# Optimization experiments

Measured on AMD Instinct MI355X. Metric: run time of the kernel, lower is better.

The kernel has to match this reference:

```python
import jax, jax.numpy as jnp
import numpy as np

BOS, EOS, MAX_STEPS = 1, 2, 50
VOCAB, EMBD, HID, CTX, SEQ = 50257, 512, 1024, 1024, 50


def setup_inputs() -> dict:
    key = jax.random.key(0)
    ks = jax.random.split(key, 13)
    s = 0.05
    return {
        "seq_enc_states": jax.random.normal(ks[0], (SEQ, 1, CTX), jnp.float32),
        "seq_enc_hidden": jax.random.normal(ks[1], (1, CTX), jnp.float32),
        "E": jax.random.normal(ks[2], (VOCAB, EMBD), jnp.float32) * s,
        "W_init": jax.random.normal(ks[3], (HID, CTX), jnp.float32) * s,
        "b_init": jax.random.normal(ks[4], (HID,), jnp.float32) * s,
        "Wa": jax.random.normal(ks[5], (CTX, HID), jnp.float32) * s,
        "ba": jax.random.normal(ks[6], (CTX,), jnp.float32) * s,
        "W_ih": jax.random.normal(ks[7], (3 * HID, EMBD + CTX), jnp.float32) * s,
        "W_hh": jax.random.normal(ks[8], (3 * HID, HID), jnp.float32) * s,
        "b_ih": jax.random.normal(ks[9], (3 * HID,), jnp.float32) * s,
        "b_hh": jax.random.normal(ks[10], (3 * HID,), jnp.float32) * s,
        "Wv": jax.random.normal(ks[11], (VOCAB, HID), jnp.float32) * s,
        "bv": jax.random.normal(ks[12], (VOCAB,), jnp.float32) * s,
    }


def _gru_cell(x, h, W_ih, W_hh, b_ih, b_hh):
    # torch.nn.GRUCell math
    gi = x @ W_ih.T + b_ih  # (1, 3H)
    gh = h @ W_hh.T + b_hh  # (1, 3H)
    i_r, i_z, i_n = jnp.split(gi, 3, axis=-1)
    h_r, h_z, h_n = jnp.split(gh, 3, axis=-1)
    r = jax.nn.sigmoid(i_r + h_r)
    z = jax.nn.sigmoid(i_z + h_z)
    n = jnp.tanh(i_n + r * h_n)
    return (1.0 - z) * n + z * h


def reference(seq_enc_states, seq_enc_hidden, E, W_init, b_init, Wa, ba,
              W_ih, W_hh, b_ih, b_hh, Wv, bv):
    enc = seq_enc_states[:, 0, :]                       # (S, CTX)
    h0 = seq_enc_hidden.reshape(1, -1) @ W_init.T + b_init  # (1, H)
    emb0 = E[BOS][None, :]                              # (1, EMBD)

    def step(carry, _):
        h, emb, done = carry
        # dot-product attention over the 50 encoder positions
        ph = h @ Wa.T + ba                              # (1, CTX)
        attn = jax.nn.softmax(ph @ enc.T, axis=-1)      # (1, S)
        ctx = attn @ enc                                # (1, CTX)
        x = jnp.concatenate([emb, ctx], axis=-1)        # (1, EMBD+CTX)
        h_new = _gru_cell(x, h, W_ih, W_hh, b_ih, b_hh)
        logp = jax.nn.log_softmax(h_new @ Wv.T + bv, axis=-1)  # (1, V)
        idx = jnp.argmax(logp[0])
        valid = jnp.logical_not(done)
        is_eos = idx == EOS
        emit_idx = jnp.where(valid & jnp.logical_not(is_eos), idx, -1).astype(jnp.int32)
        logp_out = jnp.where(valid, logp[0], 0.0)
        new_emb = jnp.where((valid & jnp.logical_not(is_eos))[..., None], E[idx][None, :], emb)
        new_h = jnp.where(valid, h_new, h)
        new_done = done | is_eos
        return (new_h, new_emb, new_done), (emit_idx, logp_out, valid)

    init = (h0, emb0, jnp.array(False))
    _, (indices, logps, valid) = jax.lax.scan(step, init, None, length=MAX_STEPS)
    # indices: (50,) int32, -1 where past eos / eos itself (not appended in original)
    return indices, logps, valid
```

## Files before the change

### kernel.cpp

```cpp
#include <hip/hip_runtime.h>
#include <hip/hip_fp8.h>
#include <cmath>

#define VOCABSZ 50257
#define EMBD 512
#define HIDD 1024
#define CTXD 1024
#define SEQL 50
#define NSTEPS 50
#define BOS_ID 1
#define EOS_ID 2

#define NTHR 256
#define NB_GH 768
#define NB_GI 768
#define NB_WR 64
#define NB_PRE (NB_GH + NB_GI + NB_WR)
#define NB_LOG 832
#define NW_LOG (NB_LOG * 4)
#define ST_STRIDE 12

#define OFF_M      0
#define OFF_T      51200
#define OFF_H      51264
#define OFF_CTX    53312
#define OFF_GI     54336
#define OFF_GH     57408
#define OFF_L      60480
#define OFF_STATS  110784
#define OFF_STATE  120768
#define OFF_WV8    120896

typedef float v2f __attribute__((ext_vector_type(2)));

__device__ __forceinline__ float wred_sum(float v) {
#pragma unroll
  for (int o = 32; o > 0; o >>= 1) v += __shfl_xor(v, o, 64);
  return v;
}

__device__ __forceinline__ float dot4(float4 a, float4 b) {
  return a.x * b.x + a.y * b.y + a.z * b.z + a.w * b.w;
}

__device__ __forceinline__ float wdot1024(const float* __restrict__ row, int lane,
                                          float4 b0, float4 b1, float4 b2, float4 b3) {
  const float4* r = (const float4*)row;
  float acc = dot4(r[lane], b0) + dot4(r[lane + 64], b1) +
              dot4(r[lane + 128], b2) + dot4(r[lane + 192], b3);
  return wred_sum(acc);
}

__device__ __forceinline__ bool beats(float v, int i, float v0, int i0) {
  return v > v0 || (v == v0 && i < i0);
}

__device__ __forceinline__ void top4_insert(float* v, int* ix, float w, int j) {
  if (!beats(w, j, v[3], ix[3])) return;
  v[3] = w; ix[3] = j;
#pragma unroll
  for (int k = 3; k > 0; --k) {
    if (beats(v[k], ix[k], v[k - 1], ix[k - 1])) {
      float tv = v[k]; v[k] = v[k - 1]; v[k - 1] = tv;
      int ti = ix[k]; ix[k] = ix[k - 1]; ix[k - 1] = ti;
    }
  }
}

#if __has_builtin(__builtin_amdgcn_cvt_pk_f32_fp8)
#define FP8_HW 1
#else
#define FP8_HW 0
__device__ __forceinline__ float fp8_sw(unsigned b) {
  unsigned s = b >> 7, e = (b >> 3) & 15, m = b & 7;
  float mag = (e == 0) ? ldexpf((float)m, -9) : ldexpf((float)(8 + m), (int)e - 10);
  return s ? -mag : mag;
}
#endif

__device__ __forceinline__ float acc16_fp8(uint4 a, const float* b) {
  float acc = 0.f;
  const unsigned dw[4] = {a.x, a.y, a.z, a.w};
#pragma unroll
  for (int d = 0; d < 4; ++d) {
#if FP8_HW
    v2f lo = __builtin_amdgcn_cvt_pk_f32_fp8((int)dw[d], false);
    v2f hi = __builtin_amdgcn_cvt_pk_f32_fp8((int)dw[d], true);
    acc += lo.x * b[d * 4 + 0] + lo.y * b[d * 4 + 1] +
           hi.x * b[d * 4 + 2] + hi.y * b[d * 4 + 3];
#else
    acc += fp8_sw(dw[d] & 0xff) * b[d * 4 + 0] +
           fp8_sw((dw[d] >> 8) & 0xff) * b[d * 4 + 1] +
           fp8_sw((dw[d] >> 16) & 0xff) * b[d * 4 + 2] +
           fp8_sw((dw[d] >> 24) & 0xff) * b[d * 4 + 3];
#endif
  }
  return acc;
}

__global__ void __launch_bounds__(NTHR)
k_cvt8(const float4* __restrict__ src, unsigned* __restrict__ dst, int n) {
  int i = blockIdx.x * NTHR + threadIdx.x;
  const int stride = gridDim.x * NTHR;
  for (; i < n; i += stride) {
    float4 v = src[i];
#if __has_builtin(__builtin_amdgcn_cvt_pk_fp8_f32)
    int p = 0;
    p = __builtin_amdgcn_cvt_pk_fp8_f32(v.x, v.y, p, false);
    p = __builtin_amdgcn_cvt_pk_fp8_f32(v.z, v.w, p, true);
    dst[i] = (unsigned)p;
#else
    __hip_fp8_e4m3 a(v.x), b(v.y), c(v.z), d(v.w);
    dst[i] = (unsigned)a.__x | ((unsigned)b.__x << 8) |
             ((unsigned)c.__x << 16) | ((unsigned)d.__x << 24);
#endif
  }
}

__global__ void __launch_bounds__(1024)
k0_matM(float* __restrict__ ws, const float* __restrict__ enc,
        const float* __restrict__ Wa) {
  const int kc = blockIdx.x;
  const int jg = blockIdx.y;
  const int tid = threadIdx.x;
  const int w = tid >> 6, lane = tid & 63;
  const int jw = w & 3, q = w >> 2;
  const int j = jg * 4 + jw;
  const int k = kc * 64 + lane;
  __shared__ float s_red[16][64];
  float acc0 = 0.f, acc1 = 0.f, acc2 = 0.f, acc3 = 0.f;
  if (j < SEQL) {
    const float4* e4 = (const float4*)(enc + (size_t)j * CTXD);
    const float* Wc = Wa + k;
    for (int c4 = q * 64; c4 < q * 64 + 64; ++c4) {
      float4 e = e4[c4];
      const float* wp = Wc + (size_t)(c4 * 4) * HIDD;
      acc0 += e.x * wp[0];
      acc1 += e.y * wp[HIDD];
      acc2 += e.z * wp[2 * HIDD];
      acc3 += e.w * wp[3 * HIDD];
    }
  }
  s_red[w][lane] = acc0 + acc1 + acc2 + acc3;
  __syncthreads();
  if (q == 0 && j < SEQL) {
    float v = s_red[jw][lane] + s_red[4 + jw][lane] +
              s_red[8 + jw][lane] + s_red[12 + jw][lane];
    ws[OFF_M + (size_t)j * HIDD + k] = v;
  }
}

__global__ void __launch_bounds__(NTHR)
k0_init(float* __restrict__ ws, const float* __restrict__ enc,
        const float* __restrict__ hid0, const float* __restrict__ Winit,
        const float* __restrict__ binit, const float* __restrict__ ba) {
  const int blk = blockIdx.x, tid = threadIdx.x;
  const int wave = tid >> 6, lane = tid & 63;
  if (blk == 0) {
    const float4* b4 = (const float4*)ba;
    float4 b0 = b4[lane], b1 = b4[lane + 64], b2 = b4[lane + 128], b3 = b4[lane + 192];
    for (int j = wave; j < SEQL; j += 4) {
      float v = wdot1024(enc + (size_t)j * CTXD, lane, b0, b1, b2, b3);
      if (lane == 0) ws[OFF_T + j] = v;
    }
    if (tid == 0) {
      int* st_emb = (int*)(ws + OFF_STATE);
      st_emb[0] = BOS_ID;
      st_emb[64] = 0;
    }
  } else {
    const float4* h4 = (const float4*)hid0;
    float4 b0 = h4[lane], b1 = h4[lane + 64], b2 = h4[lane + 128], b3 = h4[lane + 192];
    int row = (blk - 1) * 4 + wave;
    float v = wdot1024(Winit + (size_t)row * CTXD, lane, b0, b1, b2, b3) + binit[row];
    if (lane == 0) ws[OFF_H + row] = v;
  }
}

__global__ void __launch_bounds__(NTHR)
k_attn0(float* __restrict__ ws, const float* __restrict__ enc) {
  const int tid = threadIdx.x;
  const int wave = tid >> 6, lane = tid & 63;
  __shared__ float s_h[HIDD];
  __shared__ float s_sc[64], s_aw[64];
  ((float4*)s_h)[tid] = ((const float4*)(ws + OFF_H))[tid];
  __syncthreads();
  const float4* h4 = (const float4*)s_h;
  float4 b0 = h4[lane], b1 = h4[lane + 64], b2 = h4[lane + 128], b3 = h4[lane + 192];
  for (int j = wave; j < SEQL; j += 4) {
    float v = wdot1024(ws + OFF_M + (size_t)j * HIDD, lane, b0, b1, b2, b3) + ws[OFF_T + j];
    if (lane == 0) s_sc[j] = v;
  }
  __syncthreads();
  if (tid < 64) {
    float v = (tid < SEQL) ? s_sc[tid] : -INFINITY;
    float mx = v;
#pragma unroll
    for (int o = 32; o > 0; o >>= 1) mx = fmaxf(mx, __shfl_xor(mx, o, 64));
    float e = (tid < SEQL) ? expf(v - mx) : 0.f;
    float sm = wred_sum(e);
    if (tid < SEQL) s_aw[tid] = e / sm;
  }
  __syncthreads();
  const float4* enc4 = (const float4*)enc;
  float4 acc = make_float4(0.f, 0.f, 0.f, 0.f);
  for (int j = 0; j < SEQL; ++j) {
    float a = s_aw[j];
    float4 ev = enc4[(size_t)j * (CTXD / 4) + tid];
    acc.x += a * ev.x; acc.y += a * ev.y; acc.z += a * ev.z; acc.w += a * ev.w;
  }
  ((float4*)(ws + OFF_CTX))[tid] = acc;
}

__global__ void __launch_bounds__(NTHR)
k_pre(float* __restrict__ ws, const float* __restrict__ E,
      const float* __restrict__ Wih, const float* __restrict__ Whh,
      const float* __restrict__ bih, const float* __restrict__ bhh,
      const float* __restrict__ Wv, const float* __restrict__ bv,
      float* __restrict__ out, int s) {
  const int blk = blockIdx.x, tid = threadIdx.x;
  const int wave = tid >> 6, lane = tid & 63;
  int* st_emb = (int*)(ws + OFF_STATE);
  int* st_done = st_emb + 64;
  const int hoff = OFF_H + (s & 1) * HIDD;

  if (blk < NB_GH) {
    if (s >= NSTEPS) return;
    const float4* h4 = (const float4*)(ws + hoff);
    float4 b0 = h4[lane], b1 = h4[lane + 64], b2 = h4[lane + 128], b3 = h4[lane + 192];
    const int r = blk * 4 + wave;
    float v = wdot1024(Whh + (size_t)r * HIDD, lane, b0, b1, b2, b3) + bhh[r];
    if (lane == 0) ws[OFF_GH + r] = v;
    return;
  }

  const bool is_writer = (blk >= NB_GH + NB_GI);
  if (!is_writer && s >= NSTEPS) return;
  if (is_writer && s == 0) return;

  int emb_s = 0, D_s = 0, gidx = -1;
  float logZ = 0.f;
  bool valid = false, eos = false;

  if (s > 0) {
    __shared__ float rm[NTHR], rs_[NTHR];
    __shared__ float rtv[NTHR][4];
    __shared__ int rti[NTHR][4];
    __shared__ float s_ex[4];
    float m = -INFINITY, su = 0.f;
    float tv[4] = {-INFINITY, -INFINITY, -INFINITY, -INFINITY};
    int ti[4] = {0x7fffffff, 0x7fffffff, 0x7fffffff, 0x7fffffff};
    for (int q = tid; q < NB_LOG; q += NTHR) {
      const float* st = ws + OFF_STATS + (size_t)q * ST_STRIDE;
      float4 A = ((const float4*)st)[0];
      float4 B = ((const float4*)st)[1];
      float4 C = ((const float4*)st)[2];
      float mn = fmaxf(m, A.x);
      su = ((m == -INFINITY) ? 0.f : su * __expf(m - mn)) + A.y * __expf(A.x - mn);
      m = mn;
      top4_insert(tv, ti, A.z, __float_as_int(A.w));
      top4_insert(tv, ti, B.x, __float_as_int(B.y));
      top4_insert(tv, ti, B.z, __float_as_int(B.w));
      top4_insert(tv, ti, C.x, __float_as_int(C.y));
    }
    rm[tid] = m; rs_[tid] = su;
#pragma unroll
    for (int k = 0; k < 4; ++k) { rtv[tid][k] = tv[k]; rti[tid][k] = ti[k]; }
    __syncthreads();
    for (int st = 128; st > 0; st >>= 1) {
      if (tid < st) {
        float m2 = rm[tid + st], s2 = rs_[tid + st];
        float mn = fmaxf(rm[tid], m2);
        rs_[tid] = rs_[tid] * __expf(rm[tid] - mn) + s2 * __expf(m2 - mn);
        rm[tid] = mn;
        float av[4]; int ai[4];
#pragma unroll
        for (int k = 0; k < 4; ++k) { av[k] = rtv[tid][k]; ai[k] = rti[tid][k]; }
#pragma unroll
        for (int k = 0; k < 4; ++k) top4_insert(av, ai, rtv[tid + st][k], rti[tid + st][k]);
#pragma unroll
        for (int k = 0; k < 4; ++k) { rtv[tid][k] = av[k]; rti[tid][k] = ai[k]; }
      }
      __syncthreads();
    }
    const int cand = rti[0][wave];
    {
      const float4* h4 = (const float4*)(ws + hoff);
      float4 b0 = h4[lane], b1 = h4[lane + 64], b2 = h4[lane + 128], b3 = h4[lane + 192];
      float v = wdot1024(Wv + (size_t)cand * HIDD, lane, b0, b1, b2, b3) + bv[cand];
      if (lane == 0) s_ex[wave] = v;
    }
    __syncthreads();
    {
      float bb = s_ex[0]; int bi = rti[0][0];
#pragma unroll
      for (int w = 1; w < 4; ++w) {
        if (beats(s_ex[w], rti[0][w], bb, bi)) { bb = s_ex[w]; bi = rti[0][w]; }
      }
      gidx = bi;
    }
    logZ = rm[0] + logf(rs_[0]);
    const int Dp = st_done[s - 1];
    valid = (Dp == 0);
    eos = (gidx == EOS_ID);
    D_s = Dp | (eos ? 1 : 0);
    emb_s = (valid && !eos) ? gidx : st_emb[s - 1];
  } else {
    emb_s = st_emb[0];
  }

  if (!is_writer) {
    const int r = (blk - NB_GH) * 4 + wave;
    const float4* e4 = (const float4*)(E + (size_t)emb_s * EMBD);
    float4 eb0 = e4[lane], eb1 = e4[lane + 64];
    const float4* c4 = (const float4*)(ws + OFF_CTX);
    float4 cb0 = c4[lane], cb1 = c4[lane + 64], cb2 = c4[lane + 128], cb3 = c4[lane + 192];
    const float* rowp = Wih + (size_t)r * (EMBD + CTXD);
    const float4* re = (const float4*)rowp;
    const float4* rc = (const float4*)(rowp + EMBD);
    float acc = dot4(re[lane], eb0) + dot4(re[lane + 64], eb1) +
                dot4(rc[lane], cb0) + dot4(rc[lane + 64], cb1) +
                dot4(rc[lane + 128], cb2) + dot4(rc[lane + 192], cb3);
    float v = wred_sum(acc) + bih[r];
    if (lane == 0) ws[OFF_GI + r] = v;
  } else {
    if (blk == NB_GH + NB_GI && tid == 0) {
      out[s - 1] = (valid && !eos) ? (float)gidx : -1.f;
      out[NSTEPS + (size_t)NSTEPS * VOCABSZ + (s - 1)] = valid ? 1.f : 0.f;
      st_emb[s] = emb_s;
      st_done[s] = D_s;
    }
    float* logp = out + NSTEPS + (size_t)(s - 1) * VOCABSZ;
    for (int i = (blk - (NB_GH + NB_GI)) * NTHR + tid; i < VOCABSZ; i += NB_WR * NTHR)
      logp[i] = valid ? (ws[OFF_L + i] - logZ) : 0.f;
  }
}

__global__ void __launch_bounds__(NTHR)
k_logits(float* __restrict__ ws, const float* __restrict__ bv,
         const float* __restrict__ enc, int s) {
  const int blk = blockIdx.x, tid = threadIdx.x;
  const int wave = tid >> 6, lane = tid & 63;
  const int p = s & 1, np = p ^ 1;
  __shared__ float s_h[HIDD];
  __shared__ float s_sc[64], s_aw[64];
  __shared__ float swm[4], sws[4], swv[4][4];
  __shared__ int swi[4][4];

  const int* st_emb = (const int*)(ws + OFF_STATE);
  const int done = st_emb[64 + s];

  const float* hp = ws + OFF_H + p * HIDD;
#pragma unroll
  for (int it = 0; it < HIDD / NTHR; ++it) {
    const int i = tid + it * NTHR;
    float h = hp[i];
    if (done) {
      s_h[i] = h;
    } else {
      float r = 1.f / (1.f + __expf(-(ws[OFF_GI + i] + ws[OFF_GH + i])));
      float z = 1.f / (1.f + __expf(-(ws[OFF_GI + HIDD + i] + ws[OFF_GH + HIDD + i])));
      float n = tanhf(ws[OFF_GI + 2 * HIDD + i] + r * ws[OFF_GH + 2 * HIDD + i]);
      s_h[i] = (1.f - z) * n + z * h;
    }
  }
  __syncthreads();
  if (blk == 0) {
    ((float4*)(ws + OFF_H + np * HIDD))[tid] = ((const float4*)s_h)[tid];
  }

  if (blk == NB_LOG) {
    if (s + 1 < NSTEPS) {
      const float4* h4 = (const float4*)s_h;
      float4 b0 = h4[lane], b1 = h4[lane + 64], b2 = h4[lane + 128], b3 = h4[lane + 192];
      for (int j = wave; j < SEQL; j += 4) {
        float v = wdot1024(ws + OFF_M + (size_t)j * HIDD, lane, b0, b1, b2, b3) + ws[OFF_T + j];
        if (lane == 0) s_sc[j] = v;
      }
      __syncthreads();
      if (tid < 64) {
        float v = (tid < SEQL) ? s_sc[tid] : -INFINITY;
        float mx = v;
#pragma unroll
        for (int o = 32; o > 0; o >>= 1) mx = fmaxf(mx, __shfl_xor(mx, o, 64));
        float e = (tid < SEQL) ? expf(v - mx) : 0.f;
        float smv = wred_sum(e);
        if (tid < SEQL) s_aw[tid] = e / smv;
      }
      __syncthreads();
      const float4* enc4 = (const float4*)enc;
      float4 acc = make_float4(0.f, 0.f, 0.f, 0.f);
      for (int j = 0; j < SEQL; ++j) {
        float a = s_aw[j];
        float4 ev = enc4[(size_t)j * (CTXD / 4) + tid];
        acc.x += a * ev.x; acc.y += a * ev.y; acc.z += a * ev.z; acc.w += a * ev.w;
      }
      ((float4*)(ws + OFF_CTX))[tid] = acc;
    }
    return;
  }

  float hb[16];
  {
    const float4* h4 = (const float4*)s_h;
    float4 A = h4[lane * 4], B = h4[lane * 4 + 1], C = h4[lane * 4 + 2], D = h4[lane * 4 + 3];
    hb[0] = A.x; hb[1] = A.y; hb[2] = A.z; hb[3] = A.w;
    hb[4] = B.x; hb[5] = B.y; hb[6] = B.z; hb[7] = B.w;
    hb[8] = C.x; hb[9] = C.y; hb[10] = C.z; hb[11] = C.w;
    hb[12] = D.x; hb[13] = D.y; hb[14] = D.z; hb[15] = D.w;
  }
  const unsigned char* Wv8 = (const unsigned char*)(ws + OFF_WV8);
  float m = -INFINITY, sum = 0.f;
  float tv[4] = {-INFINITY, -INFINITY, -INFINITY, -INFINITY};
  int ti[4] = {0x7fffffff, 0x7fffffff, 0x7fffffff, 0x7fffffff};
  for (int row = blk * 4 + wave; row < VOCABSZ; row += NW_LOG) {
    const uint4* r4 = (const uint4*)(Wv8 + (size_t)row * HIDD);
    float acc = acc16_fp8(r4[lane], hb);
    float l = wred_sum(acc) + bv[row];
    if (lane == 0) ws[OFF_L + row] = l;
    float mn = fmaxf(m, l);
    sum = ((m == -INFINITY) ? 0.f : sum * __expf(m - mn)) + __expf(l - mn);
    m = mn;
    top4_insert(tv, ti, l, row);
  }
  if (lane == 0) {
    swm[wave] = m; sws[wave] = sum;
#pragma unroll
    for (int k = 0; k < 4; ++k) { swv[wave][k] = tv[k]; swi[wave][k] = ti[k]; }
  }
  __syncthreads();
  if (tid == 0) {
    float mm = swm[0], su = sws[0];
    float av[4]; int ai[4];
#pragma unroll
    for (int k = 0; k < 4; ++k) { av[k] = swv[0][k]; ai[k] = swi[0][k]; }
#pragma unroll
    for (int w = 1; w < 4; ++w) {
      float mn = fmaxf(mm, swm[w]);
      su = su * __expf(mm - mn) + sws[w] * __expf(swm[w] - mn);
      mm = mn;
#pragma unroll
      for (int k = 0; k < 4; ++k) top4_insert(av, ai, swv[w][k], swi[w][k]);
    }
    float* st = ws + OFF_STATS + (size_t)blk * ST_STRIDE;
    st[0] = mm; st[1] = su;
    st[2] = av[0]; st[3] = __int_as_float(ai[0]);
    st[4] = av[1]; st[5] = __int_as_float(ai[1]);
    st[6] = av[2]; st[7] = __int_as_float(ai[2]);
    st[8] = av[3]; st[9] = __int_as_float(ai[3]);
    st[10] = 0.f; st[11] = 0.f;
  }
}

extern "C" void kernel_launch(void* const* d_in, const int* in_sizes, int n_in,
                              void* d_out, int out_size, void* d_ws, size_t ws_size,
                              hipStream_t stream) {
  const float* enc   = (const float*)d_in[0];
  const float* hid0  = (const float*)d_in[1];
  const float* E     = (const float*)d_in[2];
  const float* Winit = (const float*)d_in[3];
  const float* binit = (const float*)d_in[4];
  const float* Wa    = (const float*)d_in[5];
  const float* ba    = (const float*)d_in[6];
  const float* Wih   = (const float*)d_in[7];
  const float* Whh   = (const float*)d_in[8];
  const float* bih   = (const float*)d_in[9];
  const float* bhh   = (const float*)d_in[10];
  const float* Wv    = (const float*)d_in[11];
  const float* bv    = (const float*)d_in[12];
  float* out = (float*)d_out;
  float* ws  = (float*)d_ws;

  const int n4 = (VOCABSZ * HIDD) / 4;
  k_cvt8<<<4096, NTHR, 0, stream>>>((const float4*)Wv, (unsigned*)(ws + OFF_WV8), n4);
  k0_matM<<<dim3(16, 13), 1024, 0, stream>>>(ws, enc, Wa);
  k0_init<<<257, NTHR, 0, stream>>>(ws, enc, hid0, Winit, binit, ba);
  k_attn0<<<1, NTHR, 0, stream>>>(ws, enc);
  for (int s = 0; s < NSTEPS; ++s) {
    k_pre<<<NB_PRE, NTHR, 0, stream>>>(ws, E, Wih, Whh, bih, bhh, Wv, bv, out, s);
    k_logits<<<NB_LOG + 1, NTHR, 0, stream>>>(ws, bv, enc, s);
  }
  k_pre<<<NB_PRE, NTHR, 0, stream>>>(ws, E, Wih, Whh, bih, bhh, Wv, bv, out, NSTEPS);
}
```

Before: 2.003 ms.

## Switch vocab weights to fp16 packed math and overlap W_hh GEMV with logits

Stores the vocabulary projection weights as fp16 instead of fp8 and computes logits with packed half2 FMAs, two rows per wave. Moves the hidden-to-hidden gate GEMV out of the pre-step kernel into extra blocks of the logits kernel, so it runs concurrently with the vocab projection on the freshly updated hidden state. An init kernel computes the first step's gh. This doubles weight bytes streamed per step and accumulates partial dot products in half precision, in exchange for fewer conversion instructions and one less serialized GEMV stage.

```diff
diff --git a/kernel.cpp b/kernel.cpp
--- a/kernel.cpp
+++ b/kernel.cpp
@@ -1,8 +1,9 @@
 #include <hip/hip_runtime.h>
-#include <hip/hip_fp8.h>
+#include <hip/hip_fp16.h>
 #include <cmath>
 
 #define VOCABSZ 50257
+#define NPAIRS 25129
 #define EMBD 512
 #define HIDD 1024
 #define CTXD 1024
@@ -12,12 +13,12 @@
 #define EOS_ID 2
 
 #define NTHR 256
-#define NB_GH 768
 #define NB_GI 768
 #define NB_WR 64
-#define NB_PRE (NB_GH + NB_GI + NB_WR)
+#define NB_PRE (NB_GI + NB_WR)
 #define NB_LOG 832
 #define NW_LOG (NB_LOG * 4)
+#define NB_GHN 192
 #define ST_STRIDE 12
 
 #define OFF_M      0
@@ -29,9 +30,7 @@
 #define OFF_L      60480
 #define OFF_STATS  110784
 #define OFF_STATE  120768
-#define OFF_WV8    120896
-
-typedef float v2f __attribute__((ext_vector_type(2)));
+#define OFF_WVH    120896
 
 __device__ __forceinline__ float wred_sum(float v) {
 #pragma unroll
@@ -67,53 +66,18 @@
   }
 }
 
-#if __has_builtin(__builtin_amdgcn_cvt_pk_f32_fp8)
-#define FP8_HW 1
-#else
-#define FP8_HW 0
-__device__ __forceinline__ float fp8_sw(unsigned b) {
-  unsigned s = b >> 7, e = (b >> 3) & 15, m = b & 7;
-  float mag = (e == 0) ? ldexpf((float)m, -9) : ldexpf((float)(8 + m), (int)e - 10);
-  return s ? -mag : mag;
-}
-#endif
-
-__device__ __forceinline__ float acc16_fp8(uint4 a, const float* b) {
-  float acc = 0.f;
-  const unsigned dw[4] = {a.x, a.y, a.z, a.w};
-#pragma unroll
-  for (int d = 0; d < 4; ++d) {
-#if FP8_HW
-    v2f lo = __builtin_amdgcn_cvt_pk_f32_fp8((int)dw[d], false);
-    v2f hi = __builtin_amdgcn_cvt_pk_f32_fp8((int)dw[d], true);
-    acc += lo.x * b[d * 4 + 0] + lo.y * b[d * 4 + 1] +
-           hi.x * b[d * 4 + 2] + hi.y * b[d * 4 + 3];
-#else
-    acc += fp8_sw(dw[d] & 0xff) * b[d * 4 + 0] +
-           fp8_sw((dw[d] >> 8) & 0xff) * b[d * 4 + 1] +
-           fp8_sw((dw[d] >> 16) & 0xff) * b[d * 4 + 2] +
-           fp8_sw((dw[d] >> 24) & 0xff) * b[d * 4 + 3];
-#endif
-  }
-  return acc;
-}
-
 __global__ void __launch_bounds__(NTHR)
-k_cvt8(const float4* __restrict__ src, unsigned* __restrict__ dst, int n) {
+k_cvt(const float4* __restrict__ src, uint2* __restrict__ dst, int n4) {
   int i = blockIdx.x * NTHR + threadIdx.x;
   const int stride = gridDim.x * NTHR;
-  for (; i < n; i += stride) {
+  for (; i < n4; i += stride) {
     float4 v = src[i];
-#if __has_builtin(__builtin_amdgcn_cvt_pk_fp8_f32)
-    int p = 0;
-    p = __builtin_amdgcn_cvt_pk_fp8_f32(v.x, v.y, p, false);
-    p = __builtin_amdgcn_cvt_pk_fp8_f32(v.z, v.w, p, true);
-    dst[i] = (unsigned)p;
-#else
-    __hip_fp8_e4m3 a(v.x), b(v.y), c(v.z), d(v.w);
-    dst[i] = (unsigned)a.__x | ((unsigned)b.__x << 8) |
-             ((unsigned)c.__x << 16) | ((unsigned)d.__x << 24);
-#endif
+    __half2 a = __floats2half2_rn(v.x, v.y);
+    __half2 b = __floats2half2_rn(v.z, v.w);
+    uint2 u;
+    u.x = *reinterpret_cast<unsigned*>(&a);
+    u.y = *reinterpret_cast<unsigned*>(&b);
+    dst[i] = u;
   }
 }
 
@@ -177,13 +141,11 @@
   }
 }
 
-__global__ void __launch_bounds__(NTHR)
-k_attn0(float* __restrict__ ws, const float* __restrict__ enc) {
-  const int tid = threadIdx.x;
-  const int wave = tid >> 6, lane = tid & 63;
-  __shared__ float s_h[HIDD];
-  __shared__ float s_sc[64], s_aw[64];
-  ((float4*)s_h)[tid] = ((const float4*)(ws + OFF_H))[tid];
+__device__ __forceinline__ void attn_from(float* __restrict__ ws, int hoff,
+                                          const float* __restrict__ enc,
+                                          int tid, int wave, int lane,
+                                          float* s_h, float* s_sc, float* s_aw) {
+  ((float4*)s_h)[tid] = ((const float4*)(ws + hoff))[tid];
   __syncthreads();
   const float4* h4 = (const float4*)s_h;
   float4 b0 = h4[lane], b1 = h4[lane + 64], b2 = h4[lane + 128], b3 = h4[lane + 192];
@@ -213,9 +175,26 @@
 }
 
 __global__ void __launch_bounds__(NTHR)
+k_init2(float* __restrict__ ws, const float* __restrict__ enc,
+        const float* __restrict__ Whh, const float* __restrict__ bhh) {
+  const int blk = blockIdx.x, tid = threadIdx.x;
+  const int wave = tid >> 6, lane = tid & 63;
+  if (blk == 0) {
+    __shared__ float s_h[HIDD];
+    __shared__ float s_sc[64], s_aw[64];
+    attn_from(ws, OFF_H, enc, tid, wave, lane, s_h, s_sc, s_aw);
+  } else {
+    const float4* h4 = (const float4*)(ws + OFF_H);
+    float4 b0 = h4[lane], b1 = h4[lane + 64], b2 = h4[lane + 128], b3 = h4[lane + 192];
+    const int r = (blk - 1) * 4 + wave;
+    float v = wdot1024(Whh + (size_t)r * HIDD, lane, b0, b1, b2, b3) + bhh[r];
+    if (lane == 0) ws[OFF_GH + r] = v;
+  }
+}
+
+__global__ void __launch_bounds__(NTHR)
 k_pre(float* __restrict__ ws, const float* __restrict__ E,
-      const float* __restrict__ Wih, const float* __restrict__ Whh,
-      const float* __restrict__ bih, const float* __restrict__ bhh,
+      const float* __restrict__ Wih, const float* __restrict__ bih,
       const float* __restrict__ Wv, const float* __restrict__ bv,
       float* __restrict__ out, int s) {
   const int blk = blockIdx.x, tid = threadIdx.x;
@@ -224,17 +203,7 @@
   int* st_done = st_emb + 64;
   const int hoff = OFF_H + (s & 1) * HIDD;
 
-  if (blk < NB_GH) {
-    if (s >= NSTEPS) return;
-    const float4* h4 = (const float4*)(ws + hoff);
-    float4 b0 = h4[lane], b1 = h4[lane + 64], b2 = h4[lane + 128], b3 = h4[lane + 192];
-    const int r = blk * 4 + wave;
-    float v = wdot1024(Whh + (size_t)r * HIDD, lane, b0, b1, b2, b3) + bhh[r];
-    if (lane == 0) ws[OFF_GH + r] = v;
-    return;
-  }
-
-  const bool is_writer = (blk >= NB_GH + NB_GI);
+  const bool is_writer = (blk >= NB_GI);
   if (!is_writer && s >= NSTEPS) return;
   if (is_writer && s == 0) return;
 
@@ -310,7 +279,7 @@
   }
 
   if (!is_writer) {
-    const int r = (blk - NB_GH) * 4 + wave;
+    const int r = blk * 4 + wave;
     const float4* e4 = (const float4*)(E + (size_t)emb_s * EMBD);
     float4 eb0 = e4[lane], eb1 = e4[lane + 64];
     const float4* c4 = (const float4*)(ws + OFF_CTX);
@@ -324,28 +293,26 @@
     float v = wred_sum(acc) + bih[r];
     if (lane == 0) ws[OFF_GI + r] = v;
   } else {
-    if (blk == NB_GH + NB_GI && tid == 0) {
+    if (blk == NB_GI && tid == 0) {
       out[s - 1] = (valid && !eos) ? (float)gidx : -1.f;
       out[NSTEPS + (size_t)NSTEPS * VOCABSZ + (s - 1)] = valid ? 1.f : 0.f;
       st_emb[s] = emb_s;
       st_done[s] = D_s;
     }
     float* logp = out + NSTEPS + (size_t)(s - 1) * VOCABSZ;
-    for (int i = (blk - (NB_GH + NB_GI)) * NTHR + tid; i < VOCABSZ; i += NB_WR * NTHR)
+    for (int i = (blk - NB_GI) * NTHR + tid; i < VOCABSZ; i += NB_WR * NTHR)
       logp[i] = valid ? (ws[OFF_L + i] - logZ) : 0.f;
   }
 }
 
 __global__ void __launch_bounds__(NTHR)
 k_logits(float* __restrict__ ws, const float* __restrict__ bv,
-         const float* __restrict__ enc, int s) {
+         const float* __restrict__ enc, const float* __restrict__ Whh,
+         const float* __restrict__ bhh, int s) {
   const int blk = blockIdx.x, tid = threadIdx.x;
   const int wave = tid >> 6, lane = tid & 63;
   const int p = s & 1, np = p ^ 1;
   __shared__ float s_h[HIDD];
-  __shared__ float s_sc[64], s_aw[64];
-  __shared__ float swm[4], sws[4], swv[4][4];
-  __shared__ int swi[4][4];
 
   const int* st_emb = (const int*)(ws + OFF_STATE);
   const int done = st_emb[64 + s];
@@ -369,8 +336,23 @@
     ((float4*)(ws + OFF_H + np * HIDD))[tid] = ((const float4*)s_h)[tid];
   }
 
+  if (blk > NB_LOG) {
+    if (s + 1 >= NSTEPS) return;
+    const float4* h4 = (const float4*)s_h;
+    float4 b0 = h4[lane], b1 = h4[lane + 64], b2 = h4[lane + 128], b3 = h4[lane + 192];
+    const int wid = (blk - NB_LOG - 1) * 4 + wave;
+#pragma unroll
+    for (int k = 0; k < 4; ++k) {
+      const int r = wid + 768 * k;
+      float v = wdot1024(Whh + (size_t)r * HIDD, lane, b0, b1, b2, b3) + bhh[r];
+      if (lane == 0) ws[OFF_GH + r] = v;
+    }
+    return;
+  }
+
   if (blk == NB_LOG) {
     if (s + 1 < NSTEPS) {
+      __shared__ float s_sc[64], s_aw[64];
       const float4* h4 = (const float4*)s_h;
       float4 b0 = h4[lane], b1 = h4[lane + 64], b2 = h4[lane + 128], b3 = h4[lane + 192];
       for (int j = wave; j < SEQL; j += 4) {
@@ -400,28 +382,73 @@
     return;
   }
 
-  float hb[16];
-  {
-    const float4* h4 = (const float4*)s_h;
-    float4 A = h4[lane * 4], B = h4[lane * 4 + 1], C = h4[lane * 4 + 2], D = h4[lane * 4 + 3];
-    hb[0] = A.x; hb[1] = A.y; hb[2] = A.z; hb[3] = A.w;
-    hb[4] = B.x; hb[5] = B.y; hb[6] = B.z; hb[7] = B.w;
-    hb[8] = C.x; hb[9] = C.y; hb[10] = C.z; hb[11] = C.w;
-    hb[12] = D.x; hb[13] = D.y; hb[14] = D.z; hb[15] = D.w;
-  }
-  const unsigned char* Wv8 = (const unsigned char*)(ws + OFF_WV8);
+  __shared__ float swm[4], sws[4], swv[4][4];
+  __shared__ int swi[4][4];
+  const int sub = lane & 31;
+  __half2 hb2[16];
+#pragma unroll
+  for (int k = 0; k < 4; ++k) {
+    const float* hp8 = s_h + sub * 8 + k * 256;
+#pragma unroll
+    for (int j = 0; j < 4; ++j)
+      hb2[k * 4 + j] = __floats2half2_rn(hp8[2 * j], hp8[2 * j + 1]);
+  }
+  const __half* WvH = (const __half*)(ws + OFF_WVH);
   float m = -INFINITY, sum = 0.f;
   float tv[4] = {-INFINITY, -INFINITY, -INFINITY, -INFINITY};
   int ti[4] = {0x7fffffff, 0x7fffffff, 0x7fffffff, 0x7fffffff};
-  for (int row = blk * 4 + wave; row < VOCABSZ; row += NW_LOG) {
-    const uint4* r4 = (const uint4*)(Wv8 + (size_t)row * HIDD);
-    float acc = acc16_fp8(r4[lane], hb);
-    float l = wred_sum(acc) + bv[row];
-    if (lane == 0) ws[OFF_L + row] = l;
-    float mn = fmaxf(m, l);
-    sum = ((m == -INFINITY) ? 0.f : sum * __expf(m - mn)) + __expf(l - mn);
+  const int wid = blk * 4 + wave;
+  const int myoff = (lane >= 32) ? 1 : 0;
+  for (int pr = wid; pr < NPAIRS; pr += NW_LOG) {
+    const int myrow = 2 * pr + myoff;
+    const bool vr = myrow < VOCABSZ;
+    float partial = 0.f;
+    if (vr) {
+      const uint4* r4 = (const uint4*)(WvH + (size_t)myrow * HIDD);
+      uint4 u0 = r4[sub], u1 = r4[sub + 32], u2 = r4[sub + 64], u3 = r4[sub + 96];
+      const __half2* a0 = (const __half2*)&u0;
+      const __half2* a1 = (const __half2*)&u1;
+      const __half2* a2 = (const __half2*)&u2;
+      const __half2* a3 = (const __half2*)&u3;
+      __half2 c0 = __hmul2(a0[0], hb2[0]);
+      __half2 c1 = __hmul2(a1[0], hb2[4]);
+      __half2 c2 = __hmul2(a2[0], hb2[8]);
+      __half2 c3 = __hmul2(a3[0], hb2[12]);
+#pragma unroll
+      for (int j = 1; j < 4; ++j) {
+        c0 = __hfma2(a0[j], hb2[j], c0);
+        c1 = __hfma2(a1[j], hb2[4 + j], c1);
+        c2 = __hfma2(a2[j], hb2[8 + j], c2);
+        c3 = __hfma2(a3[j], hb2[12 + j], c3);
+      }
+      __half2 cc = __hadd2(__hadd2(c0, c1), __hadd2(c2, c3));
+      float2 f = __half22float2(cc);
+      partial = f.x + f.y;
+    }
+#pragma unroll
+    for (int o = 16; o > 0; o >>= 1) partial += __shfl_xor(partial, o, 64);
+    if (vr) {
+      float l = partial + bv[myrow];
+      if (sub == 0) ws[OFF_L + myrow] = l;
+      float mn = fmaxf(m, l);
+      sum = ((m == -INFINITY) ? 0.f : sum * __expf(m - mn)) + __expf(l - mn);
+      m = mn;
+      top4_insert(tv, ti, l, myrow);
+    }
+  }
+  {
+    float m2 = __shfl_xor(m, 32, 64);
+    float s2 = __shfl_xor(sum, 32, 64);
+    float mn = fmaxf(m, m2);
+    sum = ((m == -INFINITY) ? 0.f : sum * __expf(m - mn)) +
+          ((m2 == -INFINITY) ? 0.f : s2 * __expf(m2 - mn));
     m = mn;
-    top4_insert(tv, ti, l, row);
+#pragma unroll
+    for (int k = 0; k < 4; ++k) {
+      float wv_ = __shfl_xor(tv[k], 32, 64);
+      int wi_ = __shfl_xor(ti[k], 32, 64);
+      top4_insert(tv, ti, wv_, wi_);
+    }
   }
   if (lane == 0) {
     swm[wave] = m; sws[wave] = sum;
@@ -472,13 +499,13 @@
   float* ws  = (float*)d_ws;
 
   const int n4 = (VOCABSZ * HIDD) / 4;
-  k_cvt8<<<4096, NTHR, 0, stream>>>((const float4*)Wv, (unsigned*)(ws + OFF_WV8), n4);
+  k_cvt<<<4096, NTHR, 0, stream>>>((const float4*)Wv, (uint2*)(ws + OFF_WVH), n4);
   k0_matM<<<dim3(16, 13), 1024, 0, stream>>>(ws, enc, Wa);
   k0_init<<<257, NTHR, 0, stream>>>(ws, enc, hid0, Winit, binit, ba);
-  k_attn0<<<1, NTHR, 0, stream>>>(ws, enc);
+  k_init2<<<769, NTHR, 0, stream>>>(ws, enc, Whh, bhh);
   for (int s = 0; s < NSTEPS; ++s) {
-    k_pre<<<NB_PRE, NTHR, 0, stream>>>(ws, E, Wih, Whh, bih, bhh, Wv, bv, out, s);
-    k_logits<<<NB_LOG + 1, NTHR, 0, stream>>>(ws, bv, enc, s);
-  }
-  k_pre<<<NB_PRE, NTHR, 0, stream>>>(ws, E, Wih, Whh, bih, bhh, Wv, bv, out, NSTEPS);
-}
+    k_pre<<<NB_PRE, NTHR, 0, stream>>>(ws, E, Wih, bih, Wv, bv, out, s);
+    k_logits<<<NB_LOG + 1 + NB_GHN, NTHR, 0, stream>>>(ws, bv, enc, Whh, bhh, s);
+  }
+  k_pre<<<NB_PRE, NTHR, 0, stream>>>(ws, E, Wih, bih, Wv, bv, out, NSTEPS);
+}
```

Measured after the change: 2.251 ms. +12.4%, slower.

## Move W_hh GEMV and logp writeback into logits kernel, skip finished steps

Applied to the files above, without the earlier changes.

Computes the hidden-to-hidden gate GEMV for the next step inside the logits kernel, using the freshly updated hidden state in extra blocks, with the GH buffer double-buffered. Moves the log-prob writeback for the previous step into extra blocks of the logits kernel, using a double-buffered logits array. k_pre now only computes the input-gate GEMV plus a state block, and skips work once decoding has finished. FP8 conversion is swapped for a software e4m3 encoder with x64 scaling and a bit-trick fp16-based decode. This shortens the serial critical path per step, at the cost of changed quantization numerics.

```diff
diff --git a/kernel.cpp b/kernel.cpp
--- a/kernel.cpp
+++ b/kernel.cpp
@@ -1,5 +1,5 @@
 #include <hip/hip_runtime.h>
-#include <hip/hip_fp8.h>
+#include <hip/hip_fp16.h>
 #include <cmath>
 
 #define VOCABSZ 50257
@@ -12,13 +12,20 @@
 #define EOS_ID 2
 
 #define NTHR 256
-#define NB_GH 768
 #define NB_GI 768
 #define NB_WR 64
-#define NB_PRE (NB_GH + NB_GI + NB_WR)
 #define NB_LOG 832
 #define NW_LOG (NB_LOG * 4)
+#define NB_GHN 192
 #define ST_STRIDE 12
+#define KL_ATTN NB_LOG
+#define KL_GH0 (NB_LOG + 1)
+#define KL_WR0 (NB_LOG + 1 + NB_GHN)
+#define KL_GRID (KL_WR0 + NB_WR)
+#define PRE_GRID (NB_GI + 1)
+#define PRE_GRID_FIN (NB_GI + 1 + NB_WR)
+
+#define LPAD 50304
 
 #define OFF_M      0
 #define OFF_T      51200
@@ -26,12 +33,10 @@
 #define OFF_CTX    53312
 #define OFF_GI     54336
 #define OFF_GH     57408
-#define OFF_L      60480
-#define OFF_STATS  110784
-#define OFF_STATE  120768
-#define OFF_WV8    120896
-
-typedef float v2f __attribute__((ext_vector_type(2)));
+#define OFF_L      63552
+#define OFF_STATS  164160
+#define OFF_STATE  174144
+#define OFF_WV8    174400
 
 __device__ __forceinline__ float wred_sum(float v) {
 #pragma unroll
@@ -67,53 +72,46 @@
   }
 }
 
-#if __has_builtin(__builtin_amdgcn_cvt_pk_f32_fp8)
-#define FP8_HW 1
-#else
-#define FP8_HW 0
-__device__ __forceinline__ float fp8_sw(unsigned b) {
-  unsigned s = b >> 7, e = (b >> 3) & 15, m = b & 7;
-  float mag = (e == 0) ? ldexpf((float)m, -9) : ldexpf((float)(8 + m), (int)e - 10);
-  return s ? -mag : mag;
-}
-#endif
-
-__device__ __forceinline__ float acc16_fp8(uint4 a, const float* b) {
+__device__ __forceinline__ float acc16_e4m3(uint4 a, const float* b) {
   float acc = 0.f;
   const unsigned dw[4] = {a.x, a.y, a.z, a.w};
 #pragma unroll
-  for (int d = 0; d < 4; ++d) {
-#if FP8_HW
-    v2f lo = __builtin_amdgcn_cvt_pk_f32_fp8((int)dw[d], false);
-    v2f hi = __builtin_amdgcn_cvt_pk_f32_fp8((int)dw[d], true);
-    acc += lo.x * b[d * 4 + 0] + lo.y * b[d * 4 + 1] +
-           hi.x * b[d * 4 + 2] + hi.y * b[d * 4 + 3];
-#else
-    acc += fp8_sw(dw[d] & 0xff) * b[d * 4 + 0] +
-           fp8_sw((dw[d] >> 8) & 0xff) * b[d * 4 + 1] +
-           fp8_sw((dw[d] >> 16) & 0xff) * b[d * 4 + 2] +
-           fp8_sw((dw[d] >> 24) & 0xff) * b[d * 4 + 3];
-#endif
+  for (int j = 0; j < 4; ++j) {
+    unsigned d = dw[j];
+    unsigned ue = d & 0x00FF00FFu;
+    unsigned uo = (d >> 8) & 0x00FF00FFu;
+    unsigned he = ((ue & 0x00800080u) << 8) | (((ue & 0x007F007Fu) << 7) + 0x20002000u);
+    unsigned ho = ((uo & 0x00800080u) << 8) | (((uo & 0x007F007Fu) << 7) + 0x20002000u);
+    float2 fe = __half22float2(*reinterpret_cast<__half2*>(&he));
+    float2 fo = __half22float2(*reinterpret_cast<__half2*>(&ho));
+    acc += fe.x * b[4 * j + 0] + fo.x * b[4 * j + 1] +
+           fe.y * b[4 * j + 2] + fo.y * b[4 * j + 3];
   }
   return acc;
 }
 
+__device__ __forceinline__ unsigned enc_e4m3(float x) {
+  unsigned s = (__float_as_uint(x) >> 24) & 0x80u;
+  float ax = fabsf(x);
+  if (!(ax >= 0.015625f)) return s | 0x08u;
+  int e; float fr = frexpf(ax, &e);
+  int q = (int)rintf(fr * 16.f);
+  if (q == 16) { q = 8; ++e; }
+  int E = e + 6;
+  return s | ((unsigned)E << 3) | (unsigned)(q - 8);
+}
+
 __global__ void __launch_bounds__(NTHR)
-k_cvt8(const float4* __restrict__ src, unsigned* __restrict__ dst, int n) {
+k_cvt8(const float4* __restrict__ src, unsigned* __restrict__ dst, int n4) {
   int i = blockIdx.x * NTHR + threadIdx.x;
   const int stride = gridDim.x * NTHR;
-  for (; i < n; i += stride) {
+  for (; i < n4; i += stride) {
     float4 v = src[i];
-#if __has_builtin(__builtin_amdgcn_cvt_pk_fp8_f32)
-    int p = 0;
-    p = __builtin_amdgcn_cvt_pk_fp8_f32(v.x, v.y, p, false);
-    p = __builtin_amdgcn_cvt_pk_fp8_f32(v.z, v.w, p, true);
-    dst[i] = (unsigned)p;
-#else
-    __hip_fp8_e4m3 a(v.x), b(v.y), c(v.z), d(v.w);
-    dst[i] = (unsigned)a.__x | ((unsigned)b.__x << 8) |
-             ((unsigned)c.__x << 16) | ((unsigned)d.__x << 24);
-#endif
+    unsigned b0 = enc_e4m3(v.x * 64.f);
+    unsigned b1 = enc_e4m3(v.y * 64.f);
+    unsigned b2 = enc_e4m3(v.z * 64.f);
+    unsigned b3 = enc_e4m3(v.w * 64.f);
+    dst[i] = b0 | (b1 << 8) | (b2 << 16) | (b3 << 24);
   }
 }
 
@@ -177,13 +175,11 @@
   }
 }
 
-__global__ void __launch_bounds__(NTHR)
-k_attn0(float* __restrict__ ws, const float* __restrict__ enc) {
-  const int tid = threadIdx.x;
-  const int wave = tid >> 6, lane = tid & 63;
-  __shared__ float s_h[HIDD];
-  __shared__ float s_sc[64], s_aw[64];
-  ((float4*)s_h)[tid] = ((const float4*)(ws + OFF_H))[tid];
+__device__ __forceinline__ void attn_from(float* __restrict__ ws, int hoff,
+                                          const float* __restrict__ enc,
+                                          int tid, int wave, int lane,
+                                          float* s_h, float* s_sc, float* s_aw) {
+  ((float4*)s_h)[tid] = ((const float4*)(ws + hoff))[tid];
   __syncthreads();
   const float4* h4 = (const float4*)s_h;
   float4 b0 = h4[lane], b1 = h4[lane + 64], b2 = h4[lane + 128], b3 = h4[lane + 192];
@@ -213,9 +209,26 @@
 }
 
 __global__ void __launch_bounds__(NTHR)
+k_init2(float* __restrict__ ws, const float* __restrict__ enc,
+        const float* __restrict__ Whh, const float* __restrict__ bhh) {
+  const int blk = blockIdx.x, tid = threadIdx.x;
+  const int wave = tid >> 6, lane = tid & 63;
+  if (blk == 0) {
+    __shared__ float s_h[HIDD];
+    __shared__ float s_sc[64], s_aw[64];
+    attn_from(ws, OFF_H, enc, tid, wave, lane, s_h, s_sc, s_aw);
+  } else {
+    const float4* h4 = (const float4*)(ws + OFF_H);
+    float4 b0 = h4[lane], b1 = h4[lane + 64], b2 = h4[lane + 128], b3 = h4[lane + 192];
+    const int r = (blk - 1) * 4 + wave;
+    float v = wdot1024(Whh + (size_t)r * HIDD, lane, b0, b1, b2, b3) + bhh[r];
+    if (lane == 0) ws[OFF_GH + r] = v;
+  }
+}
+
+__global__ void __launch_bounds__(NTHR)
 k_pre(float* __restrict__ ws, const float* __restrict__ E,
-      const float* __restrict__ Wih, const float* __restrict__ Whh,
-      const float* __restrict__ bih, const float* __restrict__ bhh,
+      const float* __restrict__ Wih, const float* __restrict__ bih,
       const float* __restrict__ Wv, const float* __restrict__ bv,
       float* __restrict__ out, int s) {
   const int blk = blockIdx.x, tid = threadIdx.x;
@@ -224,19 +237,11 @@
   int* st_done = st_emb + 64;
   const int hoff = OFF_H + (s & 1) * HIDD;
 
-  if (blk < NB_GH) {
-    if (s >= NSTEPS) return;
-    const float4* h4 = (const float4*)(ws + hoff);
-    float4 b0 = h4[lane], b1 = h4[lane + 64], b2 = h4[lane + 128], b3 = h4[lane + 192];
-    const int r = blk * 4 + wave;
-    float v = wdot1024(Whh + (size_t)r * HIDD, lane, b0, b1, b2, b3) + bhh[r];
-    if (lane == 0) ws[OFF_GH + r] = v;
-    return;
-  }
-
-  const bool is_writer = (blk >= NB_GH + NB_GI);
-  if (!is_writer && s >= NSTEPS) return;
-  if (is_writer && s == 0) return;
+  const bool is_gi = (blk < NB_GI);
+  const bool is_state = (blk == NB_GI);
+  const bool is_writer = (blk > NB_GI);
+  if (is_gi && s >= NSTEPS) return;
+  if ((is_state || is_writer) && s == 0) return;
 
   int emb_s = 0, D_s = 0, gidx = -1;
   float logZ = 0.f;
@@ -309,8 +314,9 @@
     emb_s = st_emb[0];
   }
 
-  if (!is_writer) {
-    const int r = (blk - NB_GH) * 4 + wave;
+  if (is_gi) {
+    if (D_s) return;
+    const int r = blk * 4 + wave;
     const float4* e4 = (const float4*)(E + (size_t)emb_s * EMBD);
     float4 eb0 = e4[lane], eb1 = e4[lane + 64];
     const float4* c4 = (const float4*)(ws + OFF_CTX);
@@ -323,34 +329,48 @@
                 dot4(rc[lane + 128], cb2) + dot4(rc[lane + 192], cb3);
     float v = wred_sum(acc) + bih[r];
     if (lane == 0) ws[OFF_GI + r] = v;
-  } else {
-    if (blk == NB_GH + NB_GI && tid == 0) {
+  } else if (is_state) {
+    if (tid == 0) {
       out[s - 1] = (valid && !eos) ? (float)gidx : -1.f;
       out[NSTEPS + (size_t)NSTEPS * VOCABSZ + (s - 1)] = valid ? 1.f : 0.f;
       st_emb[s] = emb_s;
       st_done[s] = D_s;
-    }
+      ws[OFF_STATE + 128] = logZ;
+      ws[OFF_STATE + 129] = valid ? 1.f : 0.f;
+    }
+  } else {
+    const float* Lp = ws + OFF_L + (size_t)((s - 1) & 1) * LPAD;
     float* logp = out + NSTEPS + (size_t)(s - 1) * VOCABSZ;
-    for (int i = (blk - (NB_GH + NB_GI)) * NTHR + tid; i < VOCABSZ; i += NB_WR * NTHR)
-      logp[i] = valid ? (ws[OFF_L + i] - logZ) : 0.f;
+    for (int i = (blk - NB_GI - 1) * NTHR + tid; i < VOCABSZ; i += NB_WR * NTHR)
+      logp[i] = valid ? (Lp[i] - logZ) : 0.f;
   }
 }
 
 __global__ void __launch_bounds__(NTHR)
 k_logits(float* __restrict__ ws, const float* __restrict__ bv,
-         const float* __restrict__ enc, int s) {
+         const float* __restrict__ enc, const float* __restrict__ Whh,
+         const float* __restrict__ bhh, float* __restrict__ out, int s) {
   const int blk = blockIdx.x, tid = threadIdx.x;
   const int wave = tid >> 6, lane = tid & 63;
   const int p = s & 1, np = p ^ 1;
+
+  if (blk >= KL_WR0) {
+    if (s == 0) return;
+    const float logZ = ws[OFF_STATE + 128];
+    const bool valid = ws[OFF_STATE + 129] != 0.f;
+    const float* Lp = ws + OFF_L + (size_t)np * LPAD;
+    float* logp = out + NSTEPS + (size_t)(s - 1) * VOCABSZ;
+    for (int i = (blk - KL_WR0) * NTHR + tid; i < VOCABSZ; i += NB_WR * NTHR)
+      logp[i] = valid ? (Lp[i] - logZ) : 0.f;
+    return;
+  }
+
   __shared__ float s_h[HIDD];
-  __shared__ float s_sc[64], s_aw[64];
-  __shared__ float swm[4], sws[4], swv[4][4];
-  __shared__ int swi[4][4];
-
   const int* st_emb = (const int*)(ws + OFF_STATE);
   const int done = st_emb[64 + s];
 
   const float* hp = ws + OFF_H + p * HIDD;
+  const float* ghp = ws + OFF_GH + p * 3 * HIDD;
 #pragma unroll
   for (int it = 0; it < HIDD / NTHR; ++it) {
     const int i = tid + it * NTHR;
@@ -358,9 +378,9 @@
     if (done) {
       s_h[i] = h;
     } else {
-      float r = 1.f / (1.f + __expf(-(ws[OFF_GI + i] + ws[OFF_GH + i])));
-      float z = 1.f / (1.f + __expf(-(ws[OFF_GI + HIDD + i] + ws[OFF_GH + HIDD + i])));
-      float n = tanhf(ws[OFF_GI + 2 * HIDD + i] + r * ws[OFF_GH + 2 * HIDD + i]);
+      float r = 1.f / (1.f + __expf(-(ws[OFF_GI + i] + ghp[i])));
+      float z = 1.f / (1.f + __expf(-(ws[OFF_GI + HIDD + i] + ghp[HIDD + i])));
+      float n = tanhf(ws[OFF_GI + 2 * HIDD + i] + r * ghp[2 * HIDD + i]);
       s_h[i] = (1.f - z) * n + z * h;
     }
   }
@@ -369,37 +389,54 @@
     ((float4*)(ws + OFF_H + np * HIDD))[tid] = ((const float4*)s_h)[tid];
   }
 
-  if (blk == NB_LOG) {
-    if (s + 1 < NSTEPS) {
-      const float4* h4 = (const float4*)s_h;
-      float4 b0 = h4[lane], b1 = h4[lane + 64], b2 = h4[lane + 128], b3 = h4[lane + 192];
-      for (int j = wave; j < SEQL; j += 4) {
-        float v = wdot1024(ws + OFF_M + (size_t)j * HIDD, lane, b0, b1, b2, b3) + ws[OFF_T + j];
-        if (lane == 0) s_sc[j] = v;
-      }
-      __syncthreads();
-      if (tid < 64) {
-        float v = (tid < SEQL) ? s_sc[tid] : -INFINITY;
-        float mx = v;
-#pragma unroll
-        for (int o = 32; o > 0; o >>= 1) mx = fmaxf(mx, __shfl_xor(mx, o, 64));
-        float e = (tid < SEQL) ? expf(v - mx) : 0.f;
-        float smv = wred_sum(e);
-        if (tid < SEQL) s_aw[tid] = e / smv;
-      }
-      __syncthreads();
-      const float4* enc4 = (const float4*)enc;
-      float4 acc = make_float4(0.f, 0.f, 0.f, 0.f);
-      for (int j = 0; j < SEQL; ++j) {
-        float a = s_aw[j];
-        float4 ev = enc4[(size_t)j * (CTXD / 4) + tid];
-        acc.x += a * ev.x; acc.y += a * ev.y; acc.z += a * ev.z; acc.w += a * ev.w;
-      }
-      ((float4*)(ws + OFF_CTX))[tid] = acc;
+  if (blk >= KL_GH0) {
+    if (s + 1 >= NSTEPS || done) return;
+    const float4* h4 = (const float4*)s_h;
+    float4 b0 = h4[lane], b1 = h4[lane + 64], b2 = h4[lane + 128], b3 = h4[lane + 192];
+    const int wid = (blk - KL_GH0) * 4 + wave;
+#pragma unroll
+    for (int k = 0; k < 4; ++k) {
+      const int r = wid + 768 * k;
+      float v = wdot1024(Whh + (size_t)r * HIDD, lane, b0, b1, b2, b3) + bhh[r];
+      if (lane == 0) ws[OFF_GH + np * 3 * HIDD + r] = v;
     }
     return;
   }
 
+  if (blk == KL_ATTN) {
+    if (s + 1 >= NSTEPS || done) return;
+    __shared__ float s_sc[64], s_aw[64];
+    const float4* h4 = (const float4*)s_h;
+    float4 b0 = h4[lane], b1 = h4[lane + 64], b2 = h4[lane + 128], b3 = h4[lane + 192];
+    for (int j = wave; j < SEQL; j += 4) {
+      float v = wdot1024(ws + OFF_M + (size_t)j * HIDD, lane, b0, b1, b2, b3) + ws[OFF_T + j];
+      if (lane == 0) s_sc[j] = v;
+    }
+    __syncthreads();
+    if (tid < 64) {
+      float v = (tid < SEQL) ? s_sc[tid] : -INFINITY;
+      float mx = v;
+#pragma unroll
+      for (int o = 32; o > 0; o >>= 1) mx = fmaxf(mx, __shfl_xor(mx, o, 64));
+      float e = (tid < SEQL) ? expf(v - mx) : 0.f;
+      float smv = wred_sum(e);
+      if (tid < SEQL) s_aw[tid] = e / smv;
+    }
+    __syncthreads();
+    const float4* enc4 = (const float4*)enc;
+    float4 acc = make_float4(0.f, 0.f, 0.f, 0.f);
+    for (int j = 0; j < SEQL; ++j) {
+      float a = s_aw[j];
+      float4 ev = enc4[(size_t)j * (CTXD / 4) + tid];
+      acc.x += a * ev.x; acc.y += a * ev.y; acc.z += a * ev.z; acc.w += a * ev.w;
+    }
+    ((float4*)(ws + OFF_CTX))[tid] = acc;
+    return;
+  }
+
+  if (done) return;
+  __shared__ float swm[4], sws[4], swv[4][4];
+  __shared__ int swi[4][4];
   float hb[16];
   {
     const float4* h4 = (const float4*)s_h;
@@ -410,14 +447,15 @@
     hb[12] = D.x; hb[13] = D.y; hb[14] = D.z; hb[15] = D.w;
   }
   const unsigned char* Wv8 = (const unsigned char*)(ws + OFF_WV8);
+  float* Lc = ws + OFF_L + (size_t)p * LPAD;
   float m = -INFINITY, sum = 0.f;
   float tv[4] = {-INFINITY, -INFINITY, -INFINITY, -INFINITY};
   int ti[4] = {0x7fffffff, 0x7fffffff, 0x7fffffff, 0x7fffffff};
   for (int row = blk * 4 + wave; row < VOCABSZ; row += NW_LOG) {
     const uint4* r4 = (const uint4*)(Wv8 + (size_t)row * HIDD);
-    float acc = acc16_fp8(r4[lane], hb);
-    float l = wred_sum(acc) + bv[row];
-    if (lane == 0) ws[OFF_L + row] = l;
+    float acc = acc16_e4m3(r4[lane], hb);
+    float l = wred_sum(acc) * 0.015625f + bv[row];
+    if (lane == 0) Lc[row] = l;
     float mn = fmaxf(m, l);
     sum = ((m == -INFINITY) ? 0.f : sum * __expf(m - mn)) + __expf(l - mn);
     m = mn;
@@ -475,10 +513,10 @@
   k_cvt8<<<4096, NTHR, 0, stream>>>((const float4*)Wv, (unsigned*)(ws + OFF_WV8), n4);
   k0_matM<<<dim3(16, 13), 1024, 0, stream>>>(ws, enc, Wa);
   k0_init<<<257, NTHR, 0, stream>>>(ws, enc, hid0, Winit, binit, ba);
-  k_attn0<<<1, NTHR, 0, stream>>>(ws, enc);
+  k_init2<<<769, NTHR, 0, stream>>>(ws, enc, Whh, bhh);
   for (int s = 0; s < NSTEPS; ++s) {
-    k_pre<<<NB_PRE, NTHR, 0, stream>>>(ws, E, Wih, Whh, bih, bhh, Wv, bv, out, s);
-    k_logits<<<NB_LOG + 1, NTHR, 0, stream>>>(ws, bv, enc, s);
-  }
-  k_pre<<<NB_PRE, NTHR, 0, stream>>>(ws, E, Wih, Whh, bih, bhh, Wv, bv, out, NSTEPS);
-}
+    k_pre<<<PRE_GRID, NTHR, 0, stream>>>(ws, E, Wih, bih, Wv, bv, out, s);
+    k_logits<<<KL_GRID, NTHR, 0, stream>>>(ws, bv, enc, Whh, bhh, out, s);
+  }
+  k_pre<<<PRE_GRID_FIN, NTHR, 0, stream>>>(ws, E, Wih, bih, Wv, bv, out, NSTEPS);
+}
```

Measured after the change: 2.030 ms. No clear change (+1.3%).
